# Kernel tuning notes

Hardware: AMD Instinct MI355X
Metric: run time of the kernel (lower is better)

Reference implementation:

```python
import jax, jax.numpy as jnp
import numpy as np

D_MODEL = 256
NUM_HEADS = 8
WINDOW = 7
B, H, W = 2, 56, 56


def setup_inputs() -> dict:
    key = jax.random.key(0)
    ks = jax.random.split(key, 9)
    s = D_MODEL ** -0.5
    return {
        "x": jax.random.normal(ks[0], (B, D_MODEL, H, W), jnp.float32),
        "wq": jax.random.normal(ks[1], (D_MODEL, D_MODEL), jnp.float32) * s,
        "bq": jnp.zeros((D_MODEL,), jnp.float32),
        "wk": jax.random.normal(ks[2], (D_MODEL, D_MODEL), jnp.float32) * s,
        "bk": jnp.zeros((D_MODEL,), jnp.float32),
        "wv": jax.random.normal(ks[3], (D_MODEL, D_MODEL), jnp.float32) * s,
        "bv": jnp.zeros((D_MODEL,), jnp.float32),
        "wo": jax.random.normal(ks[4], (D_MODEL, D_MODEL), jnp.float32) * s,
        "bo": jnp.zeros((D_MODEL,), jnp.float32),
    }


def _proj(x, w, b):
    # 1x1 conv == channel matmul. x: [B,C,H,W], w: [Cout,Cin], b: [Cout]
    return jnp.einsum('oc,bchw->bohw', w, x) + b[None, :, None, None]


def _windows(t, ws):
    # t: [B,h,d,H,W] -> [B,h,d,H,W,ws*ws], zero-padded sliding windows.
    # Row-major (i*ws + j) flattening matches torch unfold(3).unfold(4).view(...,-1).
    pad = ws // 2
    Hh, Ww = t.shape[-2], t.shape[-1]
    tp = jnp.pad(t, ((0, 0), (0, 0), (0, 0), (pad, pad), (pad, pad)))
    return jnp.stack([tp[..., i:i + Hh, j:j + Ww]
                      for i in range(ws) for j in range(ws)], axis=-1)


def reference(x, wq, bq, wk, bk, wv, bv, wo, bo):
    Bt, C, Hh, Ww = x.shape
    hd = C // NUM_HEADS
    scale = hd ** -0.5
    q = _proj(x, wq, bq).reshape(Bt, NUM_HEADS, hd, Hh, Ww)
    k = _proj(x, wk, bk).reshape(Bt, NUM_HEADS, hd, Hh, Ww)
    v = _proj(x, wv, bv).reshape(Bt, NUM_HEADS, hd, Hh, Ww)
    kw = _windows(k, WINDOW)  # [B,h,d,H,W,ws^2]
    vw = _windows(v, WINDOW)
    attn = jnp.einsum('bhdxy,bhdxyw->bhxyw', q, kw) * scale
    attn = jax.nn.softmax(attn, axis=-1)
    out = jnp.einsum('bhxyw,bhdxyw->bhdxy', attn, vw).reshape(Bt, C, Hh, Ww)
    return _proj(out, wo, bo)
```

## Files before the change

### kernel.cpp

```cpp
#include <hip/hip_runtime.h>
#include <cstdint>

#define NHEAD 8
#define HD 32
#define DM 256
#define HH 56
#define WWID 56
#define HW 3136
#define NB 2
#define SCALE 0.17677669529663687f

#if __has_builtin(__builtin_amdgcn_exp2f)
#define QSCALE 0.25503488f
#define EXPW(x) __builtin_amdgcn_exp2f(x)
#else
#define QSCALE SCALE
#define EXPW(x) __expf(x)
#endif

typedef _Float16 f16;
typedef __attribute__((ext_vector_type(2))) _Float16 f16x2;
typedef __attribute__((ext_vector_type(8))) _Float16 f16x8;
typedef __attribute__((ext_vector_type(4))) float floatx4;

union U16 { uint4 u; f16x2 h2[4]; f16 h[8]; };

#define GLD16(g, l) __builtin_amdgcn_global_load_lds( \
    (__attribute__((address_space(1))) void*)(g),     \
    (__attribute__((address_space(3))) void*)(l), 16, 0, 0)

#if __has_builtin(__builtin_amdgcn_update_dpp)
__device__ __forceinline__ float quad_sum(float s) {
    float t1 = __int_as_float(__builtin_amdgcn_update_dpp(
        0, __float_as_int(s), 0xB1, 0xF, 0xF, true));
    s += t1;
    float t2 = __int_as_float(__builtin_amdgcn_update_dpp(
        0, __float_as_int(s), 0x4E, 0xF, 0xF, true));
    return s + t2;
}
#else
__device__ __forceinline__ float quad_sum(float s) {
    s += __shfl_xor(s, 1);
    s += __shfl_xor(s, 2);
    return s;
}
#endif

__device__ __forceinline__ float dot8(const U16& a, const U16& b) {
    float s = __builtin_amdgcn_fdot2(a.h2[0], b.h2[0], 0.0f, false);
    s = __builtin_amdgcn_fdot2(a.h2[1], b.h2[1], s, false);
    s = __builtin_amdgcn_fdot2(a.h2[2], b.h2[2], s, false);
    s = __builtin_amdgcn_fdot2(a.h2[3], b.h2[3], s, false);
    return s;
}

__global__ __launch_bounds__(256) void prep(
    const float* __restrict__ x,
    const float* __restrict__ wq, const float* __restrict__ wk,
    const float* __restrict__ wv, const float* __restrict__ wo,
    f16* __restrict__ xT, f16* __restrict__ wcat, f16* __restrict__ wob,
    f16* __restrict__ zbuf)
{
    const int bid = blockIdx.x;
    const int t = threadIdx.x;
    if (bid < 1568) {
        __shared__ float tile[32][33];
        const int b = bid / 784, r = bid - 784 * b;
        const int ct = r / 98;
        const int p0 = (r - ct * 98) * 32, c0 = ct * 32;
        const int tx = t & 31, ty = t >> 5;
        const float* xb = x + (size_t)b * DM * HW;
        #pragma unroll
        for (int i = 0; i < 4; ++i)
            tile[ty + i * 8][tx] = xb[(size_t)(c0 + ty + i * 8) * HW + p0 + tx];
        __syncthreads();
        f16* xo = xT + (size_t)b * HW * DM;
        #pragma unroll
        for (int i = 0; i < 4; ++i)
            xo[(size_t)(p0 + ty + i * 8) * DM + c0 + tx] =
                (f16)tile[tx][ty + i * 8];
    } else {
        if (bid == 1823 && t < 4)
            ((uint4*)zbuf)[t] = make_uint4(0, 0, 0, 0);
        const int gid = (bid - 1568) * 256 + t;
        const int idx4 = gid << 2;
        const int sel = idx4 >> 16;
        const int off = idx4 & 65535;
        const float* src = sel == 0 ? wq : (sel == 1 ? wk : (sel == 2 ? wv : wo));
        f16* dst = sel < 3 ? (wcat + (sel << 16) + off) : (wob + off);
        float4 f = *(const float4*)&src[off];
        union { ushort4 u; f16 h[4]; } pk;
        pk.h[0] = (f16)f.x; pk.h[1] = (f16)f.y;
        pk.h[2] = (f16)f.z; pk.h[3] = (f16)f.w;
        *(ushort4*)dst = pk.u;
    }
}

template<int MODE>
__global__ __launch_bounds__(256) void gemm_mfma(
    const f16* __restrict__ A,
    const f16* __restrict__ Bm,
    const float* __restrict__ b0, const float* __restrict__ b1,
    const float* __restrict__ b2,
    void* __restrict__ o0, void* __restrict__ o1, void* __restrict__ o2)
{
    const int bb = blockIdx.z;
    const int n0 = blockIdx.x * 64;
    const int m0 = blockIdx.y * 128;
    const f16* Bb = Bm + (size_t)bb * HW * DM + (size_t)n0 * DM;

    __shared__ __align__(16) f16 As[2][2][128][32];
    __shared__ __align__(16) f16 Bs[2][2][64][32];

    const int t = threadIdx.x;
    const int wave = t >> 6, lane = t & 63;
    const int quad = lane >> 4, l16 = lane & 15;
    const int mw = (wave & 1) * 64, nw = (wave >> 1) * 32;

    floatx4 acc[4][2] = {};

    const int sr = t >> 2;
    const int sq = (t & 3) << 3;
    const f16* gA = A + (size_t)(m0 + sr) * DM + sq;
    const f16* gB = Bb + (size_t)sr * DM + sq;

#define STAGE(buf, k0)                                           \
    GLD16(gA + (k0),                 &As[buf][0][sr][sq]);       \
    GLD16(gA + 64 * DM + (k0),       &As[buf][0][sr + 64][sq]);  \
    GLD16(gA + (k0) + 32,            &As[buf][1][sr][sq]);       \
    GLD16(gA + 64 * DM + (k0) + 32,  &As[buf][1][sr + 64][sq]);  \
    GLD16(gB + (k0),                 &Bs[buf][0][sr][sq]);       \
    GLD16(gB + (k0) + 32,            &Bs[buf][1][sr][sq]);

    STAGE(0, 0)

    #pragma unroll
    for (int kk = 0; kk < 4; ++kk) {
        const int cur = kk & 1;
        if (kk < 3) {
            const int ko = (kk + 1) * 64;
            if (cur == 0) { STAGE(1, ko) } else { STAGE(0, ko) }
            asm volatile("s_waitcnt vmcnt(6)" ::: "memory");
        } else {
            asm volatile("s_waitcnt vmcnt(0)" ::: "memory");
        }
        __builtin_amdgcn_s_barrier();
        __builtin_amdgcn_sched_barrier(0);
        #pragma unroll
        for (int s = 0; s < 2; ++s) {
            f16x8 af[4], bf[2];
            #pragma unroll
            for (int mt = 0; mt < 4; ++mt)
                af[mt] = *(const f16x8*)&As[cur][s][mw + mt * 16 + l16][quad * 8];
            #pragma unroll
            for (int nt = 0; nt < 2; ++nt)
                bf[nt] = *(const f16x8*)&Bs[cur][s][nw + nt * 16 + l16][quad * 8];
            #pragma unroll
            for (int mt = 0; mt < 4; ++mt)
                #pragma unroll
                for (int nt = 0; nt < 2; ++nt)
                    acc[mt][nt] = __builtin_amdgcn_mfma_f32_16x16x32_f16(
                        af[mt], bf[nt], acc[mt][nt], 0, 0, 0);
        }
        asm volatile("s_waitcnt lgkmcnt(0)" ::: "memory");
        __builtin_amdgcn_sched_barrier(0);
        __builtin_amdgcn_s_barrier();
    }
#undef STAGE

    if (MODE == 0) {
        #pragma unroll
        for (int mt = 0; mt < 4; ++mt) {
            const int gm = m0 + mw + mt * 16 + quad * 4;
            const int proj = gm >> 8;
            const int c = gm & 255;
            const int h = c >> 5, d0 = c & 31;
            const float* bptr = proj == 0 ? b0 : (proj == 1 ? b1 : b2);
            f16* op = (f16*)(proj == 0 ? o0 : (proj == 1 ? o1 : o2));
            const float sc = proj == 0 ? QSCALE : 1.0f;
            const size_t base = ((size_t)(bb * NHEAD + h) * HW) * HD + d0;
            float bias[4] = {bptr[c], bptr[c + 1], bptr[c + 2], bptr[c + 3]};
            #pragma unroll
            for (int nt = 0; nt < 2; ++nt) {
                const int p = n0 + nw + nt * 16 + l16;
                union { ushort4 u; f16 h[4]; } pk;
                #pragma unroll
                for (int r = 0; r < 4; ++r)
                    pk.h[r] = (f16)((acc[mt][nt][r] + bias[r]) * sc);
                *(ushort4*)&op[base + (size_t)p * HD] = pk.u;
            }
        }
    } else {
        float* yo = (float*)o0;
        #pragma unroll
        for (int mt = 0; mt < 4; ++mt) {
            const int gc = m0 + mw + mt * 16 + quad * 4;
            #pragma unroll
            for (int r = 0; r < 4; ++r) {
                const float bias = b0[gc + r];
                #pragma unroll
                for (int nt = 0; nt < 2; ++nt) {
                    const int p = n0 + nw + nt * 16 + l16;
                    yo[(size_t)(bb * DM + gc + r) * HW + p] = acc[mt][nt][r] + bias;
                }
            }
        }
    }
}

#define HROWS 10
#define HPOS  (HROWS * WWID)
#define HPP   (HPOS + 6)

__global__ __launch_bounds__(448) void attn_win(
    const f16* __restrict__ q,
    const f16* __restrict__ k,
    const f16* __restrict__ v,
    f16* __restrict__ out,
    const f16* __restrict__ zbuf)
{
    __shared__ uint4 kh[HPP * 4];
    __shared__ uint4 vh[HPP * 4];

    const int t = threadIdx.x;
    const int tile = blockIdx.x;
    const int h = blockIdx.y, b = blockIdx.z;
    const int y0 = tile * 4;
    const size_t base = (size_t)(b * NHEAD + h) * HW * HD;
    const f16* kp = k + base;
    const f16* vp = v + base;

    #pragma unroll
    for (int it = 0; it < 5; ++it) {
        const int u = t + it * 448;
        const int pos = u >> 2, ch = u & 3;
        const int hr = pos / WWID;
        const int gx = pos - hr * WWID;
        const int gy = y0 - 3 + hr;
        const bool val = (unsigned)gy < HH;
        const size_t g = (size_t)(gy * WWID + gx) * HD + (ch << 3);
        const f16* ks = val ? kp + g : zbuf;
        const f16* vs = val ? vp + g : zbuf;
        GLD16(ks, (f16*)&kh[u + 12]);
        GLD16(vs, (f16*)&vh[u + 12]);
    }
    if (t < 48) {
        const int ps = t % 6;
        const int fi = (ps < 3 ? ps * 4 : (HPOS + ps) * 4) + ((t / 6) & 3);
        const uint4 z = make_uint4(0, 0, 0, 0);
        if (t < 24) kh[fi] = z; else vh[fi] = z;
    }
    __syncthreads();

    const int g  = t >> 2;
    const int ch = t & 3;
    const int ry = g / 28;
    const int px = g - ry * 28;
    const int x0 = px * 2;
    const int plA = ry * WWID + x0;
    const int pA = y0 * WWID + plA;
    const int tA = plA * 4 + ch;

    U16 qa, qb;
    qa.u = *(const uint4*)(q + base + (size_t)pA * HD + (ch << 3));
    qb.u = *(const uint4*)(q + base + (size_t)(pA + 1) * HD + (ch << 3));

    const uint4* kb4 = kh + tA;
    const uint4* vb4 = vh + tA;

    float inr[8];
    float cA = 0.f, cB = 0.f;
    #pragma unroll
    for (int c = 0; c < 8; ++c) {
        inr[c] = ((unsigned)(x0 + c - 3) < WWID) ? 1.0f : 0.0f;
        if (c < 7) cA += inr[c];
        if (c > 0) cB += inr[c];
    }
    float ofA[8] = {}, ofB[8] = {};
    float sumA = 7.0f * (7.0f - cA);
    float sumB = 7.0f * (7.0f - cB);

    for (int i = 0; i < 7; ++i) {
        #pragma unroll
        for (int c = 0; c < 8; ++c) {
            const int off4 = (i * WWID + c) << 2;
            U16 ku; ku.u = kb4[off4];
            U16 vu; vu.u = vb4[off4];
            if (c < 7) {
                float s = quad_sum(dot8(ku, qa));
                const float w = EXPW(s) * inr[c];
                sumA += w;
                #pragma unroll
                for (int n = 0; n < 8; ++n)
                    ofA[n] = fmaf((float)vu.h[n], w, ofA[n]);
            }
            if (c > 0) {
                float s = quad_sum(dot8(ku, qb));
                const float w = EXPW(s) * inr[c];
                sumB += w;
                #pragma unroll
                for (int n = 0; n < 8; ++n)
                    ofB[n] = fmaf((float)vu.h[n], w, ofB[n]);
            }
        }
    }

#if __has_builtin(__builtin_amdgcn_rcpf)
    const float invA = __builtin_amdgcn_rcpf(sumA);
    const float invB = __builtin_amdgcn_rcpf(sumB);
#else
    const float invA = 1.0f / sumA;
    const float invB = 1.0f / sumB;
#endif
    f16* opA = out + ((size_t)b * HW + pA) * DM + h * HD + (ch << 3);
    f16* opB = opA + DM;
    U16 oa, ob;
    #pragma unroll
    for (int n = 0; n < 8; ++n) {
        oa.h[n] = (f16)(ofA[n] * invA);
        ob.h[n] = (f16)(ofB[n] * invB);
    }
    *(uint4*)opA = oa.u;
    *(uint4*)opB = ob.u;
}

extern "C" void kernel_launch(void* const* d_in, const int* in_sizes, int n_in,
                              void* d_out, int out_size, void* d_ws, size_t ws_size,
                              hipStream_t stream) {
    const float* x  = (const float*)d_in[0];
    const float* wq = (const float*)d_in[1];
    const float* bq = (const float*)d_in[2];
    const float* wk = (const float*)d_in[3];
    const float* bk = (const float*)d_in[4];
    const float* wv = (const float*)d_in[5];
    const float* bv = (const float*)d_in[6];
    const float* wo = (const float*)d_in[7];
    const float* bo = (const float*)d_in[8];
    float* out = (float*)d_out;

    const size_t NPC = (size_t)NB * HW * DM;
    f16* xT    = (f16*)d_ws;
    f16* wcat  = xT + NPC;
    f16* wob   = wcat + 768 * 256;
    f16* qb    = wob + 256 * 256;
    f16* kb    = qb + NPC;
    f16* vb    = kb + NPC;
    f16* attnT = vb + NPC;
    f16* zbuf  = attnT + NPC;

    prep<<<1824, 256, 0, stream>>>(x, wq, wk, wv, wo, xT, wcat, wob, zbuf);
    gemm_mfma<0><<<dim3(HW / 64, 6, NB), 256, 0, stream>>>(
        wcat, xT, bq, bk, bv, qb, kb, vb);
    attn_win<<<dim3(14, NHEAD, NB), 448, 0, stream>>>(qb, kb, vb, attnT, zbuf);
    gemm_mfma<1><<<dim3(HW / 64, 2, NB), 256, 0, stream>>>(
        wob, attnT, bo, bo, bo, out, out, out);
}
```

Before: 103.4 us.

## Enlarge QKV GEMM tile to 256x64 and transpose tile to 64x64

Splits the templated GEMM into a dedicated QKV kernel that uses 256-row by 64-column tiles. Each wave now covers 64x64 with a 4x4 MFMA accumulator, so the B tile is reused across more rows and the block count drops from 6 to 3 in M. The prep transpose also moves from 32x32 to 64x64 tiles, which means fewer, larger blocks. In exchange there are fewer blocks in flight (294 GEMM blocks, 392 transpose blocks), more accumulator registers, and a larger LDS footprint per block, so occupancy may fall.

```diff
diff --git a/kernel.cpp b/kernel.cpp
--- a/kernel.cpp
+++ b/kernel.cpp
@@ -63,26 +63,26 @@
 {
     const int bid = blockIdx.x;
     const int t = threadIdx.x;
-    if (bid < 1568) {
-        __shared__ float tile[32][33];
-        const int b = bid / 784, r = bid - 784 * b;
-        const int ct = r / 98;
-        const int p0 = (r - ct * 98) * 32, c0 = ct * 32;
-        const int tx = t & 31, ty = t >> 5;
+    if (bid < 392) {
+        __shared__ float tile[64][65];
+        const int b = bid / 196, r = bid - 196 * b;
+        const int ct = r / 49;
+        const int p0 = (r - ct * 49) * 64, c0 = ct * 64;
+        const int tx = t & 63, ty = t >> 6;
         const float* xb = x + (size_t)b * DM * HW;
         #pragma unroll
-        for (int i = 0; i < 4; ++i)
-            tile[ty + i * 8][tx] = xb[(size_t)(c0 + ty + i * 8) * HW + p0 + tx];
+        for (int i = 0; i < 16; ++i)
+            tile[ty + i * 4][tx] = xb[(size_t)(c0 + ty + i * 4) * HW + p0 + tx];
         __syncthreads();
         f16* xo = xT + (size_t)b * HW * DM;
         #pragma unroll
-        for (int i = 0; i < 4; ++i)
-            xo[(size_t)(p0 + ty + i * 8) * DM + c0 + tx] =
-                (f16)tile[tx][ty + i * 8];
+        for (int i = 0; i < 16; ++i)
+            xo[(size_t)(p0 + ty + i * 4) * DM + c0 + tx] =
+                (f16)tile[tx][ty + i * 4];
     } else {
-        if (bid == 1823 && t < 4)
+        if (bid == 647 && t < 4)
             ((uint4*)zbuf)[t] = make_uint4(0, 0, 0, 0);
-        const int gid = (bid - 1568) * 256 + t;
+        const int gid = (bid - 392) * 256 + t;
         const int idx4 = gid << 2;
         const int sel = idx4 >> 16;
         const int off = idx4 & 65535;
@@ -96,13 +96,101 @@
     }
 }
 
-template<int MODE>
-__global__ __launch_bounds__(256) void gemm_mfma(
+__global__ __launch_bounds__(256) void gemm_qkv(
     const f16* __restrict__ A,
     const f16* __restrict__ Bm,
     const float* __restrict__ b0, const float* __restrict__ b1,
     const float* __restrict__ b2,
-    void* __restrict__ o0, void* __restrict__ o1, void* __restrict__ o2)
+    f16* __restrict__ o0, f16* __restrict__ o1, f16* __restrict__ o2)
+{
+    const int bb = blockIdx.z;
+    const int n0 = blockIdx.x * 64;
+    const int m0 = blockIdx.y * 256;
+    const f16* Bb = Bm + (size_t)bb * HW * DM + (size_t)n0 * DM;
+
+    __shared__ __align__(16) f16 As[2][256][32];
+    __shared__ __align__(16) f16 Bs[2][64][32];
+
+    const int t = threadIdx.x;
+    const int wave = t >> 6, lane = t & 63;
+    const int quad = lane >> 4, l16 = lane & 15;
+    const int mw = wave * 64;
+
+    floatx4 acc[4][4] = {};
+
+    const int sr = t >> 2;
+    const int sq = (t & 3) << 3;
+    const f16* gA = A + (size_t)(m0 + sr) * DM + sq;
+    const f16* gB = Bb + (size_t)sr * DM + sq;
+
+#define STAGEQ(buf, k0)                                          \
+    GLD16(gA + (k0),                  &As[buf][sr][sq]);         \
+    GLD16(gA + 64 * DM + (k0),        &As[buf][sr + 64][sq]);    \
+    GLD16(gA + 128 * DM + (k0),       &As[buf][sr + 128][sq]);   \
+    GLD16(gA + 192 * DM + (k0),       &As[buf][sr + 192][sq]);   \
+    GLD16(gB + (k0),                  &Bs[buf][sr][sq]);
+
+    STAGEQ(0, 0)
+
+    #pragma unroll
+    for (int kk = 0; kk < 8; ++kk) {
+        const int cur = kk & 1;
+        if (kk < 7) {
+            const int ko = (kk + 1) * 32;
+            if (cur == 0) { STAGEQ(1, ko) } else { STAGEQ(0, ko) }
+            asm volatile("s_waitcnt vmcnt(5)" ::: "memory");
+        } else {
+            asm volatile("s_waitcnt vmcnt(0)" ::: "memory");
+        }
+        __builtin_amdgcn_s_barrier();
+        __builtin_amdgcn_sched_barrier(0);
+        f16x8 af[4], bf[4];
+        #pragma unroll
+        for (int mt = 0; mt < 4; ++mt)
+            af[mt] = *(const f16x8*)&As[cur][mw + mt * 16 + l16][quad * 8];
+        #pragma unroll
+        for (int nt = 0; nt < 4; ++nt)
+            bf[nt] = *(const f16x8*)&Bs[cur][nt * 16 + l16][quad * 8];
+        #pragma unroll
+        for (int mt = 0; mt < 4; ++mt)
+            #pragma unroll
+            for (int nt = 0; nt < 4; ++nt)
+                acc[mt][nt] = __builtin_amdgcn_mfma_f32_16x16x32_f16(
+                    af[mt], bf[nt], acc[mt][nt], 0, 0, 0);
+        asm volatile("s_waitcnt lgkmcnt(0)" ::: "memory");
+        __builtin_amdgcn_sched_barrier(0);
+        __builtin_amdgcn_s_barrier();
+    }
+#undef STAGEQ
+
+    #pragma unroll
+    for (int mt = 0; mt < 4; ++mt) {
+        const int gm = m0 + mw + mt * 16 + quad * 4;
+        const int proj = gm >> 8;
+        const int c = gm & 255;
+        const int h = c >> 5, d0 = c & 31;
+        const float* bptr = proj == 0 ? b0 : (proj == 1 ? b1 : b2);
+        f16* op = proj == 0 ? o0 : (proj == 1 ? o1 : o2);
+        const float sc = proj == 0 ? QSCALE : 1.0f;
+        const size_t base = ((size_t)(bb * NHEAD + h) * HW) * HD + d0;
+        float bias[4] = {bptr[c], bptr[c + 1], bptr[c + 2], bptr[c + 3]};
+        #pragma unroll
+        for (int nt = 0; nt < 4; ++nt) {
+            const int p = n0 + nt * 16 + l16;
+            union { ushort4 u; f16 h[4]; } pk;
+            #pragma unroll
+            for (int r = 0; r < 4; ++r)
+                pk.h[r] = (f16)((acc[mt][nt][r] + bias[r]) * sc);
+            *(ushort4*)&op[base + (size_t)p * HD] = pk.u;
+        }
+    }
+}
+
+__global__ __launch_bounds__(256) void gemm_out(
+    const f16* __restrict__ A,
+    const f16* __restrict__ Bm,
+    const float* __restrict__ b0,
+    float* __restrict__ yo)
 {
     const int bb = blockIdx.z;
     const int n0 = blockIdx.x * 64;
@@ -168,41 +256,16 @@
     }
 #undef STAGE
 
-    if (MODE == 0) {
-        #pragma unroll
-        for (int mt = 0; mt < 4; ++mt) {
-            const int gm = m0 + mw + mt * 16 + quad * 4;
-            const int proj = gm >> 8;
-            const int c = gm & 255;
-            const int h = c >> 5, d0 = c & 31;
-            const float* bptr = proj == 0 ? b0 : (proj == 1 ? b1 : b2);
-            f16* op = (f16*)(proj == 0 ? o0 : (proj == 1 ? o1 : o2));
-            const float sc = proj == 0 ? QSCALE : 1.0f;
-            const size_t base = ((size_t)(bb * NHEAD + h) * HW) * HD + d0;
-            float bias[4] = {bptr[c], bptr[c + 1], bptr[c + 2], bptr[c + 3]};
+    #pragma unroll
+    for (int mt = 0; mt < 4; ++mt) {
+        const int gc = m0 + mw + mt * 16 + quad * 4;
+        #pragma unroll
+        for (int r = 0; r < 4; ++r) {
+            const float bias = b0[gc + r];
             #pragma unroll
             for (int nt = 0; nt < 2; ++nt) {
                 const int p = n0 + nw + nt * 16 + l16;
-                union { ushort4 u; f16 h[4]; } pk;
-                #pragma unroll
-                for (int r = 0; r < 4; ++r)
-                    pk.h[r] = (f16)((acc[mt][nt][r] + bias[r]) * sc);
-                *(ushort4*)&op[base + (size_t)p * HD] = pk.u;
-            }
-        }
-    } else {
-        float* yo = (float*)o0;
-        #pragma unroll
-        for (int mt = 0; mt < 4; ++mt) {
-            const int gc = m0 + mw + mt * 16 + quad * 4;
-            #pragma unroll
-            for (int r = 0; r < 4; ++r) {
-                const float bias = b0[gc + r];
-                #pragma unroll
-                for (int nt = 0; nt < 2; ++nt) {
-                    const int p = n0 + nw + nt * 16 + l16;
-                    yo[(size_t)(bb * DM + gc + r) * HW + p] = acc[mt][nt][r] + bias;
-                }
+                yo[(size_t)(bb * DM + gc + r) * HW + p] = acc[mt][nt][r] + bias;
             }
         }
     }
@@ -348,10 +411,10 @@
     f16* attnT = vb + NPC;
     f16* zbuf  = attnT + NPC;
 
-    prep<<<1824, 256, 0, stream>>>(x, wq, wk, wv, wo, xT, wcat, wob, zbuf);
-    gemm_mfma<0><<<dim3(HW / 64, 6, NB), 256, 0, stream>>>(
+    prep<<<648, 256, 0, stream>>>(x, wq, wk, wv, wo, xT, wcat, wob, zbuf);
+    gemm_qkv<<<dim3(HW / 64, 3, NB), 256, 0, stream>>>(
         wcat, xT, bq, bk, bv, qb, kb, vb);
     attn_win<<<dim3(14, NHEAD, NB), 448, 0, stream>>>(qb, kb, vb, attnT, zbuf);
-    gemm_mfma<1><<<dim3(HW / 64, 2, NB), 256, 0, stream>>>(
-        wob, attnT, bo, bo, bo, out, out, out);
-}
+    gemm_out<<<dim3(HW / 64, 2, NB), 256, 0, stream>>>(
+        wob, attnT, bo, out);
+}
```

After: 104.9 us. Within noise of the previous version (+1.4%).
